# Kernel optimization log

Hardware: AMD Instinct MI355X
Metric: run time of the kernel (lower is better)

## Reference

```python
import jax, jax.numpy as jnp
import numpy as np

N_NODES = 50000
N_EDGES = 800000


def _sage_conv(x, src, dst, Wl, Wr, b):
    # PyG SAGEConv (aggr='mean', root_weight=True):
    #   out_i = lin_l(mean_{j->i} x_j) + lin_r(x_i)
    msg = x[src]                                             # [E, F] gather
    agg = jax.ops.segment_sum(msg, dst, num_segments=N_NODES)
    deg = jax.ops.segment_sum(jnp.ones((msg.shape[0],), x.dtype), dst,
                              num_segments=N_NODES)
    agg = agg / jnp.maximum(deg, 1.0)[:, None]               # mean aggregation
    return agg @ Wl + x @ Wr + b


def setup_inputs() -> dict:
    key = jax.random.key(0)
    ks = jax.random.split(key, 9)
    Fin, H1, H2, Fout = 128, 256, 128, 64

    def w(k, fi, fo):
        return jax.random.normal(k, (fi, fo), jnp.float32) / np.sqrt(fi)

    return {
        "x": jax.random.normal(ks[0], (N_NODES, Fin), jnp.float32),
        "edge_index": jax.random.randint(ks[1], (2, N_EDGES), 0, N_NODES,
                                         dtype=jnp.int64),
        "Wl1": w(ks[2], Fin, H1), "Wr1": w(ks[3], Fin, H1),
        "b1": jnp.zeros((H1,), jnp.float32),
        "Wl2": w(ks[4], H1, H2), "Wr2": w(ks[5], H1, H2),
        "b2": jnp.zeros((H2,), jnp.float32),
        "Wl3": w(ks[6], H2, Fout), "Wr3": w(ks[7], H2, Fout),
        "b3": jnp.zeros((Fout,), jnp.float32),
    }


def reference(x, edge_index, Wl1, Wr1, b1, Wl2, Wr2, b2, Wl3, Wr3, b3):
    src, dst = edge_index[0], edge_index[1]
    # conv1 -> ReLU -> (dropout: identity in eval) -> conv2 -> ReLU -> conv3 -> Sigmoid
    h = jax.nn.relu(_sage_conv(x, src, dst, Wl1, Wr1, b1))
    h = jax.nn.relu(_sage_conv(h, src, dst, Wl2, Wr2, b2))
    out = jax.nn.sigmoid(_sage_conv(h, src, dst, Wl3, Wr3, b3))
    return out
```

## Files before the change

### kernel.cpp

```cpp
#include <hip/hip_runtime.h>
#include <cstddef>


using frag  = __attribute__((ext_vector_type(8))) short;
using f32x4 = __attribute__((ext_vector_type(4))) float;

constexpr int PBITS = 9;
constexpr int PSZ   = 1 << PBITS;
constexpr int PMAX  = 128;

__device__ __forceinline__ ushort f2bf(float f) {
    union { float f; unsigned u; } v; v.f = f;
    unsigned r = v.u + 0x7FFF + ((v.u >> 16) & 1);
    return (ushort)(r >> 16);
}
__device__ __forceinline__ float bf2f(ushort u) {
    union { unsigned u; float f; } v; v.u = ((unsigned)u) << 16;
    return v.f;
}


__global__ __launch_bounds__(256)
void k_pcount(const int* __restrict__ dst, int* __restrict__ pcount, int E, int P) {
    __shared__ int h[PMAX];
    int t = threadIdx.x;
    if (t < P) h[t] = 0;
    __syncthreads();
    int base = blockIdx.x * 4096;
    int n = min(4096, E - base);
    for (int i = t; i < n; i += 256)
        atomicAdd(&h[dst[base + i] >> PBITS], 1);
    __syncthreads();
    if (t < P && h[t]) atomicAdd(&pcount[t], h[t]);
}

__global__ void k_pscan(const int* __restrict__ pcount, int* __restrict__ pbase,
                        int* __restrict__ pcursor, int P) {
    if (threadIdx.x == 0) {
        int run = 0;
        for (int p = 0; p < P; ++p) { pbase[p] = run; pcursor[p] = run; run += pcount[p]; }
        pbase[P] = run;
    }
}

__global__ __launch_bounds__(256)
void k_scatter(const int* __restrict__ src, const int* __restrict__ dst,
               int* __restrict__ pcursor, unsigned* __restrict__ pairs, int E, int P) {
    __shared__ int h[PMAX];
    __shared__ int off[PMAX];
    int t = threadIdx.x;
    if (t < P) h[t] = 0;
    __syncthreads();
    int base = blockIdx.x * 4096;
    int pp[16]; int pr[16]; unsigned pk[16];
    #pragma unroll
    for (int ii = 0; ii < 16; ++ii) {
        int idx = base + ii * 256 + t;
        bool v = idx < E;
        int d = v ? dst[idx] : 0;
        int p = d >> PBITS;
        pp[ii] = v ? p : -1;
        pr[ii] = v ? atomicAdd(&h[p], 1) : 0;
        pk[ii] = v ? ((unsigned)src[idx] | ((unsigned)(d & (PSZ - 1)) << 16)) : 0u;
    }
    __syncthreads();
    if (t < P && h[t]) off[t] = atomicAdd(&pcursor[t], h[t]);
    __syncthreads();
    #pragma unroll
    for (int ii = 0; ii < 16; ++ii)
        if (pp[ii] >= 0) pairs[off[pp[ii]] + pr[ii]] = pk[ii];
}

__global__ __launch_bounds__(256)
void k_build(const unsigned* __restrict__ pairs, const int* __restrict__ pbase,
             int* __restrict__ deg, int* __restrict__ row_start,
             ushort* __restrict__ csr16, int M) {
    __shared__ int cnt[PSZ];
    __shared__ int ls[PSZ];
    __shared__ int fil[PSZ];
    __shared__ int ws[256];
    int pid = blockIdx.x;
    int t = threadIdx.x;
    int n0 = pid << PBITS;
    int L = min(PSZ, M - n0);
    int wb = pbase[pid], we = pbase[pid + 1];
    int ne = we - wb;
    for (int j = t; j < PSZ; j += 256) { cnt[j] = 0; fil[j] = 0; }
    __syncthreads();
    for (int i = t; i < ne; i += 256)
        atomicAdd(&cnt[pairs[wb + i] >> 16], 1);
    __syncthreads();
    int a = cnt[2 * t], b = cnt[2 * t + 1];
    ws[t] = a + b;
    __syncthreads();
    for (int o = 1; o < 256; o <<= 1) {
        int v = (t >= o) ? ws[t - o] : 0;
        __syncthreads();
        ws[t] += v;
        __syncthreads();
    }
    int excl = (t > 0) ? ws[t - 1] : 0;
    ls[2 * t] = excl; ls[2 * t + 1] = excl + a;
    __syncthreads();
    for (int j = t; j < L; j += 256) {
        deg[n0 + j] = cnt[j];
        row_start[n0 + j] = wb + ls[j];
    }
    for (int i = t; i < ne; i += 256) {
        unsigned pk = pairs[wb + i];
        int ln = pk >> 16;
        int pos = wb + ls[ln] + atomicAdd(&fil[ln], 1);
        csr16[pos] = (ushort)(pk & 0xFFFFu);
    }
}


__global__ void k_cvt_x(const float* __restrict__ in, ushort* __restrict__ AX, int n4) {
    int i = blockIdx.x * blockDim.x + threadIdx.x;
    if (i < n4) {
        int row = i >> 5;
        int c4  = i & 31;
        float4 v = ((const float4*)in)[i];
        ushort4 o; o.x = f2bf(v.x); o.y = f2bf(v.y); o.z = f2bf(v.z); o.w = f2bf(v.w);
        *(ushort4*)(AX + (size_t)row * 256 + 128 + c4 * 4) = o;
    }
}

struct CvtDesc {
    const float* s[6];
    ushort*      d[6];
    int K[6];
    int N[6];
    int KD[6];
    int KO[6];
};

__global__ void k_cvt_w6(CvtDesc c) {
    int wi = blockIdx.y;
    int t = blockIdx.x * blockDim.x + threadIdx.x;
    int K = c.K[wi], N = c.N[wi];
    if (t < K * N) {
        int k = t / N, n = t % N;
        c.d[wi][(size_t)n * c.KD[wi] + c.KO[wi] + k] = f2bf(c.s[wi][t]);
    }
}


template <int F, int EPI, int LDI, int LDO>
__global__ __launch_bounds__(256)
void agg_bf(const ushort* __restrict__ in, const ushort* __restrict__ csr16,
            const int* __restrict__ row_start, const int* __restrict__ deg,
            const ushort* __restrict__ u, const float* __restrict__ bias,
            void* __restrict__ out, int nN) {
    constexpr int GPL = F / 4;
    constexpr int NPB = 256 / GPL;
    int gid  = threadIdx.x / GPL;
    int li   = threadIdx.x % GPL;
    int node = blockIdx.x * NPB + gid;
    bool valid = node < nN;
    int start = valid ? row_start[node] : 0;
    int d     = valid ? deg[node] : 0;
    float a0 = 0.f, a1 = 0.f, a2 = 0.f, a3 = 0.f;

    auto gat = [&](int j) {
        int s = csr16[start + j];
        ushort4 uv = *(const ushort4*)(in + (size_t)s * LDI + li * 4);
        a0 += bf2f(uv.x); a1 += bf2f(uv.y); a2 += bf2f(uv.z); a3 += bf2f(uv.w);
    };

    int j = 0;
    for (; j + 8 <= d; j += 8) {
        gat(j); gat(j+1); gat(j+2); gat(j+3);
        gat(j+4); gat(j+5); gat(j+6); gat(j+7);
    }
    for (; j + 2 <= d; j += 2) { gat(j); gat(j+1); }
    for (; j < d; ++j) gat(j);

    if (!valid) return;
    float inv = 1.f / (float)(d > 0 ? d : 1);
    a0 *= inv; a1 *= inv; a2 *= inv; a3 *= inv;

    size_t o4 = (size_t)node * LDO + li * 4;
    if constexpr (EPI == 0) {
        ushort4 o; o.x = f2bf(a0); o.y = f2bf(a1); o.z = f2bf(a2); o.w = f2bf(a3);
        *(ushort4*)((ushort*)out + o4) = o;
    } else {
        ushort4 uv = *(const ushort4*)(u + (size_t)node * F + li * 4);
        float4 bv = *(const float4*)(bias + li * 4);
        a0 += bf2f(uv.x) + bv.x;
        a1 += bf2f(uv.y) + bv.y;
        a2 += bf2f(uv.z) + bv.z;
        a3 += bf2f(uv.w) + bv.w;
        if constexpr (EPI == 1) {
            ushort4 o;
            o.x = f2bf(fmaxf(a0, 0.f)); o.y = f2bf(fmaxf(a1, 0.f));
            o.z = f2bf(fmaxf(a2, 0.f)); o.w = f2bf(fmaxf(a3, 0.f));
            *(ushort4*)((ushort*)out + o4) = o;
        } else {
            float4 o;
            o.x = 1.f / (1.f + __expf(-a0)); o.y = 1.f / (1.f + __expf(-a1));
            o.z = 1.f / (1.f + __expf(-a2)); o.w = 1.f / (1.f + __expf(-a3));
            *(float4*)((float*)out + o4) = o;
        }
    }
}


__device__ __forceinline__ void gload16(const ushort* gp, char* lp) {
    __builtin_amdgcn_global_load_lds(
        (const __attribute__((address_space(1))) void*)gp,
        (__attribute__((address_space(3))) void*)lp, 16, 0, 0);
}

template <int BM, int BN, int K, int ACT>
__global__ __launch_bounds__(256)
void mgemm(const ushort* __restrict__ A, const ushort* __restrict__ B,
           const float* __restrict__ bias,
           ushort* __restrict__ C1, int ld1,
           ushort* __restrict__ C2, int ld2, int nsplit,
           int M, int N) {
    constexpr int NW = 4;
    constexpr int WM = 2, WN = 2;
    constexpr int MF = BM / (WM * 16);
    constexpr int NF = BN / (WN * 16);
    constexpr int NSTEP = K / 64;
    constexpr int TB = (BM + BN) * 128;
    __shared__ char lds[2 * TB];

    const int tid  = threadIdx.x;
    const int lane = tid & 63;
    const int wid  = tid >> 6;
    const int wm   = wid % WM, wn = wid / WM;
    const int bm   = blockIdx.x * BM;
    const int bn   = blockIdx.y * BN;
    const int l15  = lane & 15;
    const int lhi  = lane >> 4;
    const int lr8  = lane >> 3;
    const int lf   = lane & 7;

    auto stage = [&](int buf, int k0) {
        char* As = lds + buf * TB;
        char* Bs = As + BM * 128;
        #pragma unroll
        for (int it = 0; it < BM / (8 * NW); ++it) {
            int r0 = (it * NW + wid) * 8;
            int row = r0 + lr8;
            int gr = bm + row; if (gr >= M) gr = M - 1;
            int gfc = lf ^ (row & 7);
            gload16(A + (size_t)gr * K + k0 + gfc * 8, As + r0 * 128);
        }
        #pragma unroll
        for (int it = 0; it < BN / (8 * NW); ++it) {
            int r0 = (it * NW + wid) * 8;
            int row = r0 + lr8;
            int gfc = lf ^ (row & 7);
            gload16(B + (size_t)(bn + row) * K + k0 + gfc * 8, Bs + r0 * 128);
        }
    };

    f32x4 acc[MF][NF] = {};

    stage(0, 0);
    #pragma unroll
    for (int s = 0; s < NSTEP; ++s) {
        __syncthreads();
        if (s + 1 < NSTEP) stage((s + 1) & 1, (s + 1) * 64);
        char* As = lds + (s & 1) * TB;
        char* Bs = As + BM * 128;
        #pragma unroll
        for (int ks = 0; ks < 2; ++ks) {
            const int kb = ks * 64 + lhi * 16;
            frag a[MF], b[NF];
            #pragma unroll
            for (int mf = 0; mf < MF; ++mf) {
                int row = wm * MF * 16 + mf * 16 + l15;
                a[mf] = *(const frag*)(As + row * 128 + (kb ^ ((row & 7) << 4)));
            }
            #pragma unroll
            for (int nf = 0; nf < NF; ++nf) {
                int row = wn * NF * 16 + nf * 16 + l15;
                b[nf] = *(const frag*)(Bs + row * 128 + (kb ^ ((row & 7) << 4)));
            }
            #pragma unroll
            for (int mf = 0; mf < MF; ++mf)
                #pragma unroll
                for (int nf = 0; nf < NF; ++nf)
                    acc[mf][nf] = __builtin_amdgcn_mfma_f32_16x16x32_bf16(
                        a[mf], b[nf], acc[mf][nf], 0, 0, 0);
        }
    }

    #pragma unroll
    for (int mf = 0; mf < MF; ++mf) {
        #pragma unroll
        for (int r = 0; r < 4; ++r) {
            int gm = bm + wm * MF * 16 + mf * 16 + lhi * 4 + r;
            if (gm >= M) continue;
            #pragma unroll
            for (int nf = 0; nf < NF; ++nf) {
                int gn = bn + wn * NF * 16 + nf * 16 + l15;
                float v = acc[mf][nf][r];
                if (bias) v += bias[gn];
                if (ACT == 1) v = fmaxf(v, 0.f);
                ushort o = f2bf(v);
                if (gn < nsplit) C1[(size_t)gm * ld1 + gn] = o;
                else             C2[(size_t)gm * ld2 + (gn - nsplit)] = o;
            }
        }
    }
}


extern "C" void kernel_launch(void* const* d_in, const int* in_sizes, int n_in,
                              void* d_out, int out_size, void* d_ws, size_t ws_size,
                              hipStream_t stream) {
    const float* x   = (const float*)d_in[0];
    const int*   ei  = (const int*)d_in[1];
    const float* Wl1 = (const float*)d_in[2];
    const float* Wr1 = (const float*)d_in[3];
    const float* b1  = (const float*)d_in[4];
    const float* Wl2 = (const float*)d_in[5];
    const float* Wr2 = (const float*)d_in[6];
    const float* b2  = (const float*)d_in[7];
    const float* Wl3 = (const float*)d_in[8];
    const float* Wr3 = (const float*)d_in[9];
    const float* b3  = (const float*)d_in[10];

    const int M = in_sizes[0] / 128;
    const int E = in_sizes[1] / 2;
    const int P = (M + PSZ - 1) / PSZ;
    const int* src = ei;
    const int* dst = ei + E;

    char* w = (char*)d_ws;
    auto alloc = [&](size_t bytes) -> void* {
        void* p = (void*)w;
        w += (bytes + 255) & ~(size_t)255;
        return p;
    };
    int* pcount    = (int*)alloc((size_t)PMAX * 4);
    int* pbase     = (int*)alloc((size_t)(PMAX + 1) * 4);
    int* pcursor   = (int*)alloc((size_t)PMAX * 4);
    unsigned* pairs = (unsigned*)alloc((size_t)E * 4);
    ushort* csr16  = (ushort*)alloc((size_t)E * 2);
    int* deg       = (int*)alloc((size_t)M * 4);
    int* row_start = (int*)alloc((size_t)M * 4);
    ushort* Wcat1T = (ushort*)alloc(256 * 256 * 2);
    ushort* Wcat2T = (ushort*)alloc(256 * 256 * 2);
    ushort* Wcat3T = (ushort*)alloc(128 * 128 * 2);
    ushort* AX   = (ushort*)alloc((size_t)M * 256 * 2);
    ushort* bufA = (ushort*)alloc((size_t)M * 128 * 2);
    ushort* bufB = (ushort*)alloc((size_t)M * 128 * 2);
    ushort* bufH = (ushort*)alloc((size_t)M * 256 * 2);
    ushort* bufC = (ushort*)alloc((size_t)M * 128 * 2);
    (void)ws_size; (void)n_in; (void)out_size;

    ushort* t2 = bufA; ushort* t3 = bufA;
    ushort* h2 = bufB;
    ushort* h1 = bufH;
    ushort* u2 = bufC;   ushort* u3 = bufC;

    hipMemsetAsync(pcount, 0, (size_t)PMAX * 4, stream);
    const int nchunk = (E + 4095) / 4096;
    k_pcount<<<nchunk, 256, 0, stream>>>(dst, pcount, E, P);
    k_pscan<<<1, 64, 0, stream>>>(pcount, pbase, pcursor, P);
    k_scatter<<<nchunk, 256, 0, stream>>>(src, dst, pcursor, pairs, E, P);
    k_build<<<P, 256, 0, stream>>>(pairs, pbase, deg, row_start, csr16, M);

    k_cvt_x<<<(M * 128 / 4 + 255) / 256, 256, 0, stream>>>(x, AX, M * 128 / 4);
    CvtDesc cd;
    cd.s[0] = Wl1; cd.d[0] = Wcat1T;           cd.K[0] = 128; cd.N[0] = 256; cd.KD[0] = 256; cd.KO[0] = 0;
    cd.s[1] = Wr1; cd.d[1] = Wcat1T;           cd.K[1] = 128; cd.N[1] = 256; cd.KD[1] = 256; cd.KO[1] = 128;
    cd.s[2] = Wl2; cd.d[2] = Wcat2T;           cd.K[2] = 256; cd.N[2] = 128; cd.KD[2] = 256; cd.KO[2] = 0;
    cd.s[3] = Wr2; cd.d[3] = Wcat2T + 128*256; cd.K[3] = 256; cd.N[3] = 128; cd.KD[3] = 256; cd.KO[3] = 0;
    cd.s[4] = Wl3; cd.d[4] = Wcat3T;           cd.K[4] = 128; cd.N[4] = 64;  cd.KD[4] = 128; cd.KO[4] = 0;
    cd.s[5] = Wr3; cd.d[5] = Wcat3T + 64*128;  cd.K[5] = 128; cd.N[5] = 64;  cd.KD[5] = 128; cd.KO[5] = 0;
    k_cvt_w6<<<dim3(128, 6), 256, 0, stream>>>(cd);

    const int gm64 = (M + 63) / 64;
    const int ga128 = (M + 7) / 8;
    const int ga64  = (M + 15) / 16;

    agg_bf<128, 0, 256, 256><<<ga128, 256, 0, stream>>>(
        AX + 128, csr16, row_start, deg, nullptr, nullptr, AX, M);
    mgemm<64, 64, 256, 1><<<dim3(gm64, 4), 256, 0, stream>>>(
        AX, Wcat1T, b1, h1, 256, h1, 256, 256, M, 256);

    mgemm<64, 64, 256, 0><<<dim3(gm64, 4), 256, 0, stream>>>(
        h1, Wcat2T, nullptr, t2, 128, u2, 128, 128, M, 256);
    agg_bf<128, 1, 128, 128><<<ga128, 256, 0, stream>>>(
        t2, csr16, row_start, deg, u2, b2, h2, M);

    mgemm<64, 64, 128, 0><<<dim3(gm64, 2), 256, 0, stream>>>(
        h2, Wcat3T, nullptr, t3, 64, u3, 64, 64, M, 128);
    agg_bf<64, 2, 64, 64><<<ga64, 256, 0, stream>>>(
        t3, csr16, row_start, deg, u3, b3, (float*)d_out, M);
}
```

Measured before the change: 211.1 us.

## Assign one wavefront per node in aggregation and merge conversion kernels

The mean-aggregation kernel now maps one 64-lane wavefront to each destination node. Lanes are split into several edge groups that gather different neighbours in parallel, and their partial sums are combined with xor shuffles. The intent is more memory-level parallelism per node and less serial latency per edge, at the cost of idle lanes and extra shuffles for low-degree nodes. The x and weight bf16 conversion kernels are also merged into one launch to cut launch overhead.

```diff
diff --git a/kernel.cpp b/kernel.cpp
--- a/kernel.cpp
+++ b/kernel.cpp
@@ -115,17 +115,6 @@
 }
 
 
-__global__ void k_cvt_x(const float* __restrict__ in, ushort* __restrict__ AX, int n4) {
-    int i = blockIdx.x * blockDim.x + threadIdx.x;
-    if (i < n4) {
-        int row = i >> 5;
-        int c4  = i & 31;
-        float4 v = ((const float4*)in)[i];
-        ushort4 o; o.x = f2bf(v.x); o.y = f2bf(v.y); o.z = f2bf(v.z); o.w = f2bf(v.w);
-        *(ushort4*)(AX + (size_t)row * 256 + 128 + c4 * 4) = o;
-    }
-}
-
 struct CvtDesc {
     const float* s[6];
     ushort*      d[6];
@@ -135,13 +124,27 @@
     int KO[6];
 };
 
-__global__ void k_cvt_w6(CvtDesc c) {
-    int wi = blockIdx.y;
-    int t = blockIdx.x * blockDim.x + threadIdx.x;
-    int K = c.K[wi], N = c.N[wi];
-    if (t < K * N) {
-        int k = t / N, n = t % N;
-        c.d[wi][(size_t)n * c.KD[wi] + c.KO[wi] + k] = f2bf(c.s[wi][t]);
+__global__ void k_cvt_all(CvtDesc c, const float* __restrict__ x,
+                          ushort* __restrict__ AX, int n4, int xblocks) {
+    int bid = blockIdx.x;
+    if (bid < xblocks) {
+        int i = bid * 256 + threadIdx.x;
+        if (i < n4) {
+            int row = i >> 5;
+            int c4  = i & 31;
+            float4 v = ((const float4*)x)[i];
+            ushort4 o; o.x = f2bf(v.x); o.y = f2bf(v.y); o.z = f2bf(v.z); o.w = f2bf(v.w);
+            *(ushort4*)(AX + (size_t)row * 256 + 128 + c4 * 4) = o;
+        }
+    } else {
+        int wb = bid - xblocks;
+        int wi = wb >> 7;
+        int t = (wb & 127) * 256 + threadIdx.x;
+        int K = c.K[wi], N = c.N[wi];
+        if (t < K * N) {
+            int k = t / N, n = t % N;
+            c.d[wi][(size_t)n * c.KD[wi] + c.KO[wi] + k] = f2bf(c.s[wi][t]);
+        }
     }
 }
 
@@ -153,13 +156,14 @@
             const ushort* __restrict__ u, const float* __restrict__ bias,
             void* __restrict__ out, int nN) {
     constexpr int GPL = F / 4;
-    constexpr int NPB = 256 / GPL;
-    int gid  = threadIdx.x / GPL;
-    int li   = threadIdx.x % GPL;
-    int node = blockIdx.x * NPB + gid;
-    bool valid = node < nN;
-    int start = valid ? row_start[node] : 0;
-    int d     = valid ? deg[node] : 0;
+    constexpr int EPW = 64 / GPL;
+    int lane = threadIdx.x & 63;
+    int li   = lane & (GPL - 1);
+    int ei   = lane / GPL;
+    int node = blockIdx.x * 4 + (threadIdx.x >> 6);
+    if (node >= nN) return;
+    int start = row_start[node];
+    int d = deg[node];
     float a0 = 0.f, a1 = 0.f, a2 = 0.f, a3 = 0.f;
 
     auto gat = [&](int j) {
@@ -169,14 +173,21 @@
     };
 
     int j = 0;
-    for (; j + 8 <= d; j += 8) {
-        gat(j); gat(j+1); gat(j+2); gat(j+3);
-        gat(j+4); gat(j+5); gat(j+6); gat(j+7);
-    }
-    for (; j + 2 <= d; j += 2) { gat(j); gat(j+1); }
-    for (; j < d; ++j) gat(j);
-
-    if (!valid) return;
+    for (; j + 4 * EPW <= d; j += 4 * EPW) {
+        gat(j + ei); gat(j + EPW + ei); gat(j + 2 * EPW + ei); gat(j + 3 * EPW + ei);
+    }
+    for (; j + EPW <= d; j += EPW) gat(j + ei);
+    if (j + ei < d) gat(j + ei);
+
+    #pragma unroll
+    for (int off = GPL; off < 64; off <<= 1) {
+        a0 += __shfl_xor(a0, off);
+        a1 += __shfl_xor(a1, off);
+        a2 += __shfl_xor(a2, off);
+        a3 += __shfl_xor(a3, off);
+    }
+    if (ei != 0) return;
+
     float inv = 1.f / (float)(d > 0 ? d : 1);
     a0 *= inv; a1 *= inv; a2 *= inv; a3 *= inv;
 
@@ -367,7 +378,6 @@
     k_scatter<<<nchunk, 256, 0, stream>>>(src, dst, pcursor, pairs, E, P);
     k_build<<<P, 256, 0, stream>>>(pairs, pbase, deg, row_start, csr16, M);
 
-    k_cvt_x<<<(M * 128 / 4 + 255) / 256, 256, 0, stream>>>(x, AX, M * 128 / 4);
     CvtDesc cd;
     cd.s[0] = Wl1; cd.d[0] = Wcat1T;           cd.K[0] = 128; cd.N[0] = 256; cd.KD[0] = 256; cd.KO[0] = 0;
     cd.s[1] = Wr1; cd.d[1] = Wcat1T;           cd.K[1] = 128; cd.N[1] = 256; cd.KD[1] = 256; cd.KO[1] = 128;
@@ -375,24 +385,25 @@
     cd.s[3] = Wr2; cd.d[3] = Wcat2T + 128*256; cd.K[3] = 256; cd.N[3] = 128; cd.KD[3] = 256; cd.KO[3] = 0;
     cd.s[4] = Wl3; cd.d[4] = Wcat3T;           cd.K[4] = 128; cd.N[4] = 64;  cd.KD[4] = 128; cd.KO[4] = 0;
     cd.s[5] = Wr3; cd.d[5] = Wcat3T + 64*128;  cd.K[5] = 128; cd.N[5] = 64;  cd.KD[5] = 128; cd.KO[5] = 0;
-    k_cvt_w6<<<dim3(128, 6), 256, 0, stream>>>(cd);
+    const int n4 = M * 128 / 4;
+    const int xblocks = (n4 + 255) / 256;
+    k_cvt_all<<<xblocks + 6 * 128, 256, 0, stream>>>(cd, x, AX, n4, xblocks);
 
     const int gm64 = (M + 63) / 64;
-    const int ga128 = (M + 7) / 8;
-    const int ga64  = (M + 15) / 16;
-
-    agg_bf<128, 0, 256, 256><<<ga128, 256, 0, stream>>>(
+    const int gagg = (M + 3) / 4;
+
+    agg_bf<128, 0, 256, 256><<<gagg, 256, 0, stream>>>(
         AX + 128, csr16, row_start, deg, nullptr, nullptr, AX, M);
     mgemm<64, 64, 256, 1><<<dim3(gm64, 4), 256, 0, stream>>>(
         AX, Wcat1T, b1, h1, 256, h1, 256, 256, M, 256);
 
     mgemm<64, 64, 256, 0><<<dim3(gm64, 4), 256, 0, stream>>>(
         h1, Wcat2T, nullptr, t2, 128, u2, 128, 128, M, 256);
-    agg_bf<128, 1, 128, 128><<<ga128, 256, 0, stream>>>(
+    agg_bf<128, 1, 128, 128><<<gagg, 256, 0, stream>>>(
         t2, csr16, row_start, deg, u2, b2, h2, M);
 
     mgemm<64, 64, 128, 0><<<dim3(gm64, 2), 256, 0, stream>>>(
         h2, Wcat3T, nullptr, t3, 64, u3, 64, 64, M, 128);
-    agg_bf<64, 2, 64, 64><<<ga64, 256, 0, stream>>>(
+    agg_bf<64, 2, 64, 64><<<gagg, 256, 0, stream>>>(
         t3, csr16, row_start, deg, u3, b3, (float*)d_out, M);
 }
```

New measurement: 225.2 us. +6.7%, slower.
